# Optimization experiments

Hardware: AMD Instinct MI355X
Metric: run time of the kernel (lower is better)

Reference implementation:

```python
import jax, jax.numpy as jnp
import numpy as np

NUM_SENSORS = 32
STATE_DIM = 2
OBS_DIM = 2 * NUM_SENSORS
T = 4096
LOG2PI = float(np.log(2.0 * np.pi))


def setup_inputs() -> dict:
    key = jax.random.key(0)
    k1, = jax.random.split(key, 1)
    track = jax.random.normal(k1, (T, OBS_DIM), dtype=jnp.float32)
    bias_scales = jnp.ones((2,), dtype=jnp.float32)          # nn.Parameter(torch.ones(2))
    obs_noise = jnp.ones((), dtype=jnp.float32)              # nn.Parameter(torch.tensor(1.0))
    trans_noise = jnp.ones((1,), dtype=jnp.float32)          # nn.Parameter(torch.ones(1))
    transition_param = jnp.ones((2,), dtype=jnp.float32)     # used in forward (diag_embed().flip(0))
    return {
        "track": track,
        "bias_scales": bias_scales,
        "obs_noise": obs_noise,
        "trans_noise": trans_noise,
        "transition_param": transition_param,
    }


def reference(track, bias_scales, obs_noise, trans_noise, transition_param):
    # Gaussian HMM marginal log-likelihood, identical to the funsor sum-product:
    # bias ~ N(0, diag(tile(bias_scales, S)))  (covariance given directly)
    # state_init ~ N(0, I_2)
    # state_t = A^T state_{t-1} + eps,  eps ~ N(0, trans_noise^2 I_2)
    #   with A = diag(transition_param).flip(0), loc = prev @ A = A^T prev
    # obs_t = H^T state_t + bias + nu,  nu ~ N(0, obs_noise^2 I_obs)
    # Bias is folded into an augmented state z = [state, bias] and the whole
    # recursion is a Kalman forward filter (exact marginalization = logaddexp
    # sum-product over Gaussians).
    S = NUM_SENSORS
    sd = STATE_DIM
    od = 2 * S
    d = sd + od

    A = jnp.flip(jnp.diag(transition_param), 0)              # diag_embed().flip(0)
    F_state = A.T                                            # curr_loc = prev @ A
    F = (jnp.zeros((d, d), dtype=track.dtype)
         .at[:sd, :sd].set(F_state)
         .at[sd:, sd:].set(jnp.eye(od, dtype=track.dtype)))  # bias persists
    q = trans_noise[0] ** 2                                  # scale_tril diag -> var
    Q = jnp.zeros((d, d), dtype=track.dtype).at[:sd, :sd].set(q * jnp.eye(sd, dtype=track.dtype))

    # observation_matrix: eye(2).expand(S,2,2).transpose(0,-1).reshape(2, od)
    Ht = jnp.repeat(jnp.eye(sd, dtype=track.dtype), S, axis=0)        # (od, sd)
    C = jnp.concatenate([Ht, jnp.eye(od, dtype=track.dtype)], axis=1)  # (od, d)
    R = (obs_noise ** 2) * jnp.eye(od, dtype=track.dtype)

    bias_var = jnp.tile(bias_scales, S)                      # expand(S,2).reshape(-1)
    P0 = (jnp.zeros((d, d), dtype=track.dtype)
          .at[:sd, :sd].set(jnp.eye(sd, dtype=track.dtype))  # init_dist cov = I_2
          .at[sd:, sd:].set(jnp.diag(bias_var)))
    m0 = jnp.zeros((d,), dtype=track.dtype)

    def step(carry, y):
        m, P, ll = carry
        # predict
        m = F @ m
        P = F @ P @ F.T + Q
        # update
        mu = C @ m
        Smat = C @ P @ C.T + R                               # (od, od)
        L = jnp.linalg.cholesky(Smat)
        r = y - mu
        alpha = jax.scipy.linalg.cho_solve((L, True), r)
        ll = ll + (-0.5 * jnp.dot(r, alpha)
                   - jnp.sum(jnp.log(jnp.diagonal(L)))
                   - 0.5 * od * LOG2PI)
        CP = C @ P                                           # (od, d)
        K = jax.scipy.linalg.cho_solve((L, True), CP).T      # (d, od)
        m = m + K @ r
        P = P - K @ CP
        P = 0.5 * (P + P.T)                                  # keep symmetric
        return (m, P, ll), None

    init = (m0, P0, jnp.zeros((), dtype=track.dtype))
    (_, _, ll), _ = jax.lax.scan(step, init, track)
    return ll
```

## Files before the change

### kernel.cpp

```cpp
#include <hip/hip_runtime.h>

#define TT 4096
#define LOG2PI 1.8378770664093453


struct MRed {
    float a00, a01, a10, a11;
    float b0a, b0b, b1a, b1b;
    float c0, cx, c1;
    float j00, j01, j11;
    float ja, jb, jc, jd;
    float p4d, p4o, p4x, p4e, p4f;
};

struct DRed {
    float g00, g01, g10, g11;
    float ga00, ga01, ga10, ga11;
    float d0a, d0b, d1a, d1b;
    float gc00, gc01, gc10, gc11;
    float clev;
};

struct Elem { float b0, b1, h0, h1, h2, h3, h4, h5, g; };

__device__ __forceinline__ DRed derive(const MRed& M, bool want_clev) {
    DRed D;
    const float cj00 = M.c0 * M.j00 + M.cx * M.j01;
    const float cj01 = M.c0 * M.j01 + M.cx * M.j11;
    const float cj10 = M.cx * M.j00 + M.c1 * M.j01;
    const float cj11 = M.cx * M.j01 + M.c1 * M.j11;
    const float m00 = 1.f + cj00, m01 = cj01, m10 = cj10, m11 = 1.f + cj11;
    const float det = m00 * m11 - m01 * m10;
    const float id = 1.f / det;
    D.g00 = m11 * id; D.g01 = -m01 * id; D.g10 = -m10 * id; D.g11 = m00 * id;
    D.clev = want_clev ? (-0.5f * logf(det)) : 0.f;
    const float CJa0 = M.c0 * M.ja + M.cx * M.jc, CJa1 = M.cx * M.ja + M.c1 * M.jc;
    const float CJb0 = M.c0 * M.jb + M.cx * M.jd, CJb1 = M.cx * M.jb + M.c1 * M.jd;
    const float g0a = -(D.g00 * CJa0 + D.g01 * CJa1);
    const float g1a = -(D.g10 * CJa0 + D.g11 * CJa1);
    const float g0b = -(D.g00 * CJb0 + D.g01 * CJb1);
    const float g1b = -(D.g10 * CJb0 + D.g11 * CJb1);
    D.ga00 = D.g00 * M.a00 + D.g01 * M.a10; D.ga01 = D.g00 * M.a01 + D.g01 * M.a11;
    D.ga10 = D.g10 * M.a00 + D.g11 * M.a10; D.ga11 = D.g10 * M.a01 + D.g11 * M.a11;
    D.d0a = D.g00 * M.b0a + D.g01 * M.b1a + g0a;
    D.d1a = D.g10 * M.b0a + D.g11 * M.b1a + g1a;
    D.d0b = D.g00 * M.b0b + D.g01 * M.b1b + g0b;
    D.d1b = D.g10 * M.b0b + D.g11 * M.b1b + g1b;
    D.gc00 = D.g00 * M.c0 + D.g01 * M.cx; D.gc01 = D.g00 * M.cx + D.g01 * M.c1;
    D.gc10 = D.g10 * M.c0 + D.g11 * M.cx; D.gc11 = D.g10 * M.cx + D.g11 * M.c1;
    return D;
}

__device__ __forceinline__ void mupdate(MRed& M, const DRed& D) {
    const float k00 = M.j00 * D.ga00 + M.j01 * D.ga10, k01 = M.j00 * D.ga01 + M.j01 * D.ga11;
    const float k10 = M.j01 * D.ga00 + M.j11 * D.ga10, k11 = M.j01 * D.ga01 + M.j11 * D.ga11;
    const float V0a = M.j00 * D.d0a + M.j01 * D.d1a + M.ja;
    const float V1a = M.j01 * D.d0a + M.j11 * D.d1a + M.jc;
    const float V0b = M.j00 * D.d0b + M.j01 * D.d1b + M.jb;
    const float V1b = M.j01 * D.d0b + M.j11 * D.d1b + M.jd;
    const float U0a = M.a00 * V0a + M.a10 * V1a, U1a = M.a01 * V0a + M.a11 * V1a;
    const float U0b = M.a00 * V0b + M.a10 * V1b, U1b = M.a01 * V0b + M.a11 * V1b;
    const float Ta0 = M.b0a * k00 + M.b1a * k10 + M.ja * D.ga00 + M.jc * D.ga10;
    const float Ta1 = M.b0a * k01 + M.b1a * k11 + M.ja * D.ga01 + M.jc * D.ga11;
    const float Tb0 = M.b0b * k00 + M.b1b * k10 + M.jb * D.ga00 + M.jd * D.ga10;
    const float Tb1 = M.b0b * k01 + M.b1b * k11 + M.jb * D.ga01 + M.jd * D.ga11;
    const float Eaa = M.b0a * V0a + M.b1a * V1a + M.ja * D.d0a + M.jc * D.d1a;
    const float Eab = M.b0a * V0b + M.b1a * V1b + M.ja * D.d0b + M.jc * D.d1b;
    const float Eba = M.b0b * V0a + M.b1b * V1a + M.jb * D.d0a + M.jd * D.d1a;
    const float Ebb = M.b0b * V0b + M.b1b * V1b + M.jb * D.d0b + M.jd * D.d1b;
    const float nj00 = M.j00 + (M.a00 * k00 + M.a10 * k10);
    const float nj11 = M.j11 + (M.a01 * k01 + M.a11 * k11);
    const float nj01 = M.j01 + 0.5f * ((M.a00 * k01 + M.a10 * k11) + (M.a01 * k00 + M.a11 * k10));
    const float nja = M.ja + 0.5f * (U0a + Ta0);
    const float njc = M.jc + 0.5f * (U1a + Ta1);
    const float njb = M.jb + 0.5f * (U0b + Tb0);
    const float njd = M.jd + 0.5f * (U1b + Tb1);
    const float np4d = M.p4d + Eaa, np4o = M.p4o + Eaa;
    const float np4x = M.p4x + 0.5f * (Eab + Eba);
    const float np4e = M.p4e + Ebb, np4f = M.p4f + Ebb;
    const float ta = M.a00 * D.gc00 + M.a01 * D.gc10, tb = M.a00 * D.gc01 + M.a01 * D.gc11;
    const float tc = M.a10 * D.gc00 + M.a11 * D.gc10, td = M.a10 * D.gc01 + M.a11 * D.gc11;
    const float X00 = ta * M.a00 + tb * M.a01, X01 = ta * M.a10 + tb * M.a11;
    const float X10 = tc * M.a00 + td * M.a01, X11 = tc * M.a10 + td * M.a11;
    const float nc0 = M.c0 + X00, ncx = M.cx + 0.5f * (X01 + X10), nc1 = M.c1 + X11;
    const float na00 = M.a00 * D.ga00 + M.a01 * D.ga10, na01 = M.a00 * D.ga01 + M.a01 * D.ga11;
    const float na10 = M.a10 * D.ga00 + M.a11 * D.ga10, na11 = M.a10 * D.ga01 + M.a11 * D.ga11;
    const float nb0a = M.a00 * D.d0a + M.a01 * D.d1a + M.b0a;
    const float nb1a = M.a10 * D.d0a + M.a11 * D.d1a + M.b1a;
    const float nb0b = M.a00 * D.d0b + M.a01 * D.d1b + M.b0b;
    const float nb1b = M.a10 * D.d0b + M.a11 * D.d1b + M.b1b;
    M.a00 = na00; M.a01 = na01; M.a10 = na10; M.a11 = na11;
    M.b0a = nb0a; M.b0b = nb0b; M.b1a = nb1a; M.b1b = nb1b;
    M.c0 = nc0; M.cx = ncx; M.c1 = nc1;
    M.j00 = nj00; M.j01 = nj01; M.j11 = nj11;
    M.ja = nja; M.jb = njb; M.jc = njc; M.jd = njd;
    M.p4d = np4d; M.p4o = np4o; M.p4x = np4x; M.p4e = np4e; M.p4f = np4f;
}

__device__ __forceinline__ Elem shfl_elem(const Elem& e, int src) {
    Elem r;
    r.b0 = __shfl(e.b0, src, 64); r.b1 = __shfl(e.b1, src, 64);
    r.h0 = __shfl(e.h0, src, 64); r.h1 = __shfl(e.h1, src, 64);
    r.h2 = __shfl(e.h2, src, 64); r.h3 = __shfl(e.h3, src, 64);
    r.h4 = __shfl(e.h4, src, 64); r.h5 = __shfl(e.h5, src, 64);
    r.g  = __shfl(e.g,  src, 64);
    return r;
}

__device__ __forceinline__ Elem compose_red(const MRed& M, const DRed& D,
                                            const Elem& e1, const Elem& e2) {
    const float Jb0 = M.j00 * e1.b0 + M.j01 * e1.b1;
    const float Jb1 = M.j01 * e1.b0 + M.j11 * e1.b1;
    const float Jba = M.ja * e1.b0 + M.jc * e1.b1;
    const float Jbb = M.jb * e1.b0 + M.jd * e1.b1;
    const float Gb0 = D.g00 * e1.b0 + D.g01 * e1.b1;
    const float Gb1 = D.g10 * e1.b0 + D.g11 * e1.b1;
    const float t0 = e1.b0 + M.c0 * e2.h0 + M.cx * e2.h1;
    const float t1 = e1.b1 + M.cx * e2.h0 + M.c1 * e2.h1;
    const float u0 = D.g00 * t0 + D.g01 * t1;
    const float u1 = D.g10 * t0 + D.g11 * t1;
    Elem o;
    o.b0 = M.a00 * u0 + M.a01 * u1 + e2.b0;
    o.b1 = M.a10 * u0 + M.a11 * u1 + e2.b1;
    const float w0 = e2.h0 - Jb0, w1 = e2.h1 - Jb1;
    const float w2 = e2.h2 - Jba, w3 = e2.h3 - Jba;
    const float w4 = e2.h4 - Jbb, w5 = e2.h5 - Jbb;
    o.h0 = e1.h0 + w0 * D.ga00 + w1 * D.ga10;
    o.h1 = e1.h1 + w0 * D.ga01 + w1 * D.ga11;
    o.h2 = e1.h2 + w0 * D.d0a + w1 * D.d1a + w2;
    o.h3 = e1.h3 + w0 * D.d0a + w1 * D.d1a + w3;
    o.h4 = e1.h4 + w0 * D.d0b + w1 * D.d1b + w4;
    o.h5 = e1.h5 + w0 * D.d0b + w1 * D.d1b + w5;
    const float q1 = Jb0 * Gb0 + Jb1 * Gb1;
    const float bil = e2.h0 * Gb0 + e2.h1 * Gb1;
    const float q2 = e2.h0 * (D.gc00 * e2.h0 + D.gc01 * e2.h1)
                   + e2.h1 * (D.gc10 * e2.h0 + D.gc11 * e2.h1);
    o.g = e1.g + e2.g + D.clev - 0.5f * q1 + bil + 0.5f * q2;
    return o;
}

__device__ __forceinline__ MRed m_init(float a0, float a1, float q, float rr,
                                       float& c, float& kpp, float& glc) {
    c = 16.f * q / (rr * (rr + 32.f * q));
    const float s2 = 1.f / rr - 2.f * c;
    kpp = 4.f * q * s2;
    const float om8 = 1.f - 8.f * kpp;
    glc = 2.f * (float)LOG2PI + logf(rr) + logf(rr + 32.f * q);
    MRed M;
    M.a00 = 0.f; M.a01 = om8 * a0; M.a10 = om8 * a1; M.a11 = 0.f;
    M.b0a = -kpp; M.b0b = 0.f; M.b1a = 0.f; M.b1b = -kpp;
    M.c0 = om8 * q; M.cx = 0.f; M.c1 = om8 * q;
    M.j00 = 32.f * a1 * a1 * s2; M.j01 = 0.f; M.j11 = 32.f * a0 * a0 * s2;
    M.ja = 0.f; M.jb = 4.f * a1 * s2; M.jc = 4.f * a0 * s2; M.jd = 0.f;
    const float Sd = 1.f / rr - c, So = -c;
    M.p4d = Sd; M.p4o = So; M.p4x = 0.f; M.p4e = Sd; M.p4f = So;
    return M;
}

__global__ __launch_bounds__(256) void leaf_kernel(const float* __restrict__ track,
                                                   float* __restrict__ ws,
                                                   const float* __restrict__ obs_noise,
                                                   const float* __restrict__ trans_noise,
                                                   const float* __restrict__ tp) {
    __shared__ float zp[256];
    __shared__ float sqp[16], syp[16];
    __shared__ float4 ybar_s[64];
    const int tid = threadIdx.x, w = tid >> 6, l = tid & 63, b = blockIdx.x;
    const float a0 = tp[0], a1 = tp[1];
    const float q = trans_noise[0] * trans_noise[0];
    const float rr = obs_noise[0] * obs_noise[0];
    const float* base = track + (size_t)b * 64 * 64;
    const int g = ((l >> 5) << 1) | (l & 1);
    const bool writer = (l == 0) || (l == 1) || (l == 32) || (l == 33);
    float accz = 0.f, accsq = 0.f, accy2 = 0.f;
#pragma unroll
    for (int it = 0; it < 16; ++it) {
        const int tl = it * 4 + w;
        const float v = base[tl * 64 + l];
        accz += v; accsq += v * v;
        float s = v;
        s += __shfl_xor(s, 2, 64); s += __shfl_xor(s, 4, 64);
        s += __shfl_xor(s, 8, 64); s += __shfl_xor(s, 16, 64);
        if (writer) {
            const float yb = 0.25f * s;
            ((float*)&ybar_s[tl])[g] = yb;
            accy2 += yb * yb;
        }
    }
    zp[tid] = accz;
    float s2 = accsq;
    s2 += __shfl_xor(s2, 2, 64); s2 += __shfl_xor(s2, 4, 64);
    s2 += __shfl_xor(s2, 8, 64); s2 += __shfl_xor(s2, 16, 64);
    if (writer) { sqp[w * 4 + g] = s2; syp[w * 4 + g] = accy2; }
    __syncthreads();
    if (w != 0) return;

    float* slot = ws + b * 96;
    slot[l] = zp[l] + zp[64 + l] + zp[128 + l] + zp[192 + l];
    if (l < 4) {
        slot[64 + l] = sqp[l] + sqp[4 + l] + sqp[8 + l] + sqp[12 + l];
    } else if (l < 8) {
        const int gg = l - 4;
        slot[68 + gg] = syp[gg] + syp[4 + gg] + syp[8 + gg] + syp[12 + gg];
    }

    float c, kpp, glc;
    MRed M = m_init(a0, a1, q, rr, c, kpp, glc);
    const float4 y = ybar_s[l];
    const float irr = 1.f / rr;
    const float bs0 = y.x + y.y, bs1 = y.z + y.w;
    const float v0 = y.x * irr - c * bs0, v1 = y.y * irr - c * bs0;
    const float v2 = y.z * irr - c * bs1, v3 = y.w * irr - c * bs1;
    Elem e;
    e.b0 = kpp * bs0; e.b1 = kpp * bs1;
    e.h0 = 4.f * a1 * (v2 + v3); e.h1 = 4.f * a0 * (v0 + v1);
    e.h2 = v0; e.h3 = v1; e.h4 = v2; e.h5 = v3;
    e.g = -0.5f * (y.x * v0 + y.y * v1 + y.z * v2 + y.w * v3) - glc;

#pragma unroll
    for (int k = 0; k < 6; ++k) {
        const DRed D = derive(M, true);
        const int sA = (2 * l) & 63, sB = (2 * l + 1) & 63;
        const Elem e1 = shfl_elem(e, sA);
        const Elem e2 = shfl_elem(e, sB);
        e = compose_red(M, D, e1, e2);
        mupdate(M, D);
    }
    if (l == 0) {
        float4* eo = (float4*)(slot + 72);
        eo[0] = make_float4(e.b0, e.b1, e.h0, e.h1);
        eo[1] = make_float4(e.h2, e.h3, e.h4, e.h5);
        eo[2] = make_float4(e.g, 0.f, 0.f, 0.f);
    }
}

__global__ __launch_bounds__(64) void final_kernel(const float* __restrict__ ws,
                                                   const float* __restrict__ bias_scales,
                                                   const float* __restrict__ obs_noise,
                                                   const float* __restrict__ trans_noise,
                                                   const float* __restrict__ tp,
                                                   float* __restrict__ out) {
    __shared__ float cst[16];
    const int l = threadIdx.x;
    const float a0 = tp[0], a1 = tp[1];
    const float q = trans_noise[0] * trans_noise[0];
    const float rr = obs_noise[0] * obs_noise[0];
    const float bsc0 = bias_scales[0], bsc1 = bias_scales[1];
    float c, kpp, glc;
    MRed M = m_init(a0, a1, q, rr, c, kpp, glc);
#pragma unroll
    for (int k = 0; k < 6; ++k) { const DRed D = derive(M, false); mupdate(M, D); }

    float zacc = 0.f;
#pragma unroll 8
    for (int b = 0; b < 64; ++b) zacc += ws[b * 96 + l];
    float aux = 0.f;
    if (l < 8) {
        const int off = 64 + l;
#pragma unroll 8
        for (int b = 0; b < 64; ++b) aux += ws[b * 96 + off];
    }

    const float4* ep = (const float4*)(ws + l * 96 + 72);
    const float4 p0 = ep[0], p1 = ep[1], p2 = ep[2];
    Elem e;
    e.b0 = p0.x; e.b1 = p0.y;
    e.h0 = p0.z; e.h1 = p0.w; e.h2 = p1.x; e.h3 = p1.y; e.h4 = p1.z; e.h5 = p1.w;
    e.g = p2.x;

#pragma unroll
    for (int k = 0; k < 6; ++k) {
        const DRed D = derive(M, true);
        const int sA = (2 * l) & 63, sB = (2 * l + 1) & 63;
        const Elem e1 = shfl_elem(e, sA);
        const Elem e2 = shfl_elem(e, sB);
        e = compose_red(M, D, e1, e2);
        mupdate(M, D);
    }

    float sz = zacc, sz2 = zacc * zacc;
    sz += __shfl_xor(sz, 2, 64);  sz2 += __shfl_xor(sz2, 2, 64);
    sz += __shfl_xor(sz, 4, 64);  sz2 += __shfl_xor(sz2, 4, 64);
    sz += __shfl_xor(sz, 8, 64);  sz2 += __shfl_xor(sz2, 8, 64);
    sz += __shfl_xor(sz, 16, 64); sz2 += __shfl_xor(sz2, 16, 64);
    const int g = ((l >> 5) << 1) | (l & 1);
    if (l == 0 || l == 1 || l == 32 || l == 33) { cst[g] = sz; cst[4 + g] = sz2; }
    if (l < 8) cst[8 + l] = aux;
    __syncthreads();

    if (l == 0) {
        float J6[6][6];
        J6[0][0] = M.j00; J6[0][1] = J6[1][0] = M.j01; J6[1][1] = M.j11;
        J6[0][2] = J6[0][3] = J6[2][0] = J6[3][0] = M.ja;
        J6[0][4] = J6[0][5] = J6[4][0] = J6[5][0] = M.jb;
        J6[1][2] = J6[1][3] = J6[2][1] = J6[3][1] = M.jc;
        J6[1][4] = J6[1][5] = J6[4][1] = J6[5][1] = M.jd;
        J6[2][2] = J6[3][3] = M.p4d; J6[2][3] = J6[3][2] = M.p4o;
        J6[2][4] = J6[2][5] = J6[3][4] = J6[3][5] = M.p4x;
        J6[4][2] = J6[5][2] = J6[4][3] = J6[5][3] = M.p4x;
        J6[4][4] = J6[5][5] = M.p4e; J6[4][5] = J6[5][4] = M.p4f;
        const float s[6] = {1.f, 1.f, sqrtf(bsc0), sqrtf(bsc1), sqrtf(bsc0), sqrtf(bsc1)};
        float Mm[6][6];
#pragma unroll
        for (int i = 0; i < 6; ++i)
#pragma unroll
            for (int j = 0; j < 6; ++j)
                Mm[i][j] = ((i == j) ? 1.f : 0.f) + s[i] * s[j] * J6[i][j];
        float Lo[6][6];
#pragma unroll
        for (int i = 0; i < 6; ++i) {
#pragma unroll
            for (int j = 0; j <= i; ++j) {
                float sum = Mm[i][j];
#pragma unroll
                for (int m = 0; m < 6; ++m) if (m < j) sum -= Lo[i][m] * Lo[j][m];
                if (i == j) Lo[i][i] = sqrtf(sum);
                else Lo[i][j] = sum / Lo[j][j];
            }
        }
        float ldet = 0.f;
#pragma unroll
        for (int i = 0; i < 6; ++i) ldet += logf(Lo[i][i]);
        ldet *= 2.f;
        const float hr[6] = {e.h0, e.h1, e.h2, e.h3, e.h4, e.h5};
        float yv[6];
#pragma unroll
        for (int i = 0; i < 6; ++i) {
            float sum = s[i] * hr[i];
#pragma unroll
            for (int m = 0; m < 6; ++m) if (m < i) sum -= Lo[i][m] * yv[m];
            yv[i] = sum / Lo[i][i];
        }
        float qd = 0.f;
#pragma unroll
        for (int i = 0; i < 6; ++i) qd += yv[i] * yv[i];
        double llc = (double)e.g - 0.5 * (double)ldet + 0.5 * (double)qd;

        const float bgv[4] = {bsc0, bsc1, bsc0, bsc1};
        const double r = (double)rr;
        const double T_ = 4096.0;
#pragma unroll
        for (int gg = 0; gg < 4; ++gg) {
            const double b = (double)bgv[gg];
            const double sumz = (double)cst[gg];
            const double sumz2 = (double)cst[4 + gg];
            const double Zp = sumz2 - sumz * sumz / 16.0;
            const double Sqp = (double)cst[8 + gg] - (double)cst[12 + gg];
            llc += -0.5 * Sqp / r
                   + 0.5 * (b / (r * (r + T_ * b))) * Zp
                   - 7.5 * ((T_ - 1.0) * log(r) + log(r + T_ * b))
                   - 7.5 * T_ * LOG2PI;
        }
        out[0] = (float)llc;
    }
}

extern "C" void kernel_launch(void* const* d_in, const int* in_sizes, int n_in,
                              void* d_out, int out_size, void* d_ws, size_t ws_size,
                              hipStream_t stream) {
    const float* track            = (const float*)d_in[0];
    const float* bias_scales      = (const float*)d_in[1];
    const float* obs_noise        = (const float*)d_in[2];
    const float* trans_noise      = (const float*)d_in[3];
    const float* transition_param = (const float*)d_in[4];
    float* ws = (float*)d_ws;
    float* out = (float*)d_out;

    leaf_kernel<<<64, 256, 0, stream>>>(track, ws, obs_noise, trans_noise, transition_param);
    final_kernel<<<1, 64, 0, stream>>>(ws, bias_scales, obs_noise, trans_noise,
                                       transition_param, out);
}
```

Before: 83.90 us.

## Fuse leaf and final kernels using last-block atomic counter

Merges the two launches into one kernel. Each block writes its partial results, then increments a global counter, and the last block to arrive runs the final reduction and scan. The final block now reads the auxiliary sums as float4 loads and reduces them with wave shuffles instead of a serial loop, and the shared-memory staging of the constants becomes register shuffles. A memset of the counter is added on the stream, so the kernel-launch gap is swapped for a memset plus atomic and fence overhead.

Result: no change. 82.97 us (-1.1%).

```diff
diff --git a/kernel.cpp b/kernel.cpp
--- a/kernel.cpp
+++ b/kernel.cpp
@@ -157,14 +157,18 @@
     return M;
 }
 
-__global__ __launch_bounds__(256) void leaf_kernel(const float* __restrict__ track,
-                                                   float* __restrict__ ws,
-                                                   const float* __restrict__ obs_noise,
-                                                   const float* __restrict__ trans_noise,
-                                                   const float* __restrict__ tp) {
+__global__ __launch_bounds__(256) void fused_kernel(const float* __restrict__ track,
+                                                    float* __restrict__ ws,
+                                                    int* __restrict__ counter,
+                                                    const float* __restrict__ bias_scales,
+                                                    const float* __restrict__ obs_noise,
+                                                    const float* __restrict__ trans_noise,
+                                                    const float* __restrict__ tp,
+                                                    float* __restrict__ out) {
     __shared__ float zp[256];
     __shared__ float sqp[16], syp[16];
     __shared__ float4 ybar_s[64];
+    __shared__ int is_last;
     const int tid = threadIdx.x, w = tid >> 6, l = tid & 63, b = blockIdx.x;
     const float a0 = tp[0], a1 = tp[1];
     const float q = trans_noise[0] * trans_noise[0];
@@ -193,102 +197,95 @@
     s2 += __shfl_xor(s2, 8, 64); s2 += __shfl_xor(s2, 16, 64);
     if (writer) { sqp[w * 4 + g] = s2; syp[w * 4 + g] = accy2; }
     __syncthreads();
-    if (w != 0) return;
-
-    float* slot = ws + b * 96;
-    slot[l] = zp[l] + zp[64 + l] + zp[128 + l] + zp[192 + l];
-    if (l < 4) {
-        slot[64 + l] = sqp[l] + sqp[4 + l] + sqp[8 + l] + sqp[12 + l];
-    } else if (l < 8) {
-        const int gg = l - 4;
-        slot[68 + gg] = syp[gg] + syp[4 + gg] + syp[8 + gg] + syp[12 + gg];
-    }
 
     float c, kpp, glc;
     MRed M = m_init(a0, a1, q, rr, c, kpp, glc);
-    const float4 y = ybar_s[l];
-    const float irr = 1.f / rr;
-    const float bs0 = y.x + y.y, bs1 = y.z + y.w;
-    const float v0 = y.x * irr - c * bs0, v1 = y.y * irr - c * bs0;
-    const float v2 = y.z * irr - c * bs1, v3 = y.w * irr - c * bs1;
-    Elem e;
-    e.b0 = kpp * bs0; e.b1 = kpp * bs1;
-    e.h0 = 4.f * a1 * (v2 + v3); e.h1 = 4.f * a0 * (v0 + v1);
-    e.h2 = v0; e.h3 = v1; e.h4 = v2; e.h5 = v3;
-    e.g = -0.5f * (y.x * v0 + y.y * v1 + y.z * v2 + y.w * v3) - glc;
-
-#pragma unroll
-    for (int k = 0; k < 6; ++k) {
-        const DRed D = derive(M, true);
-        const int sA = (2 * l) & 63, sB = (2 * l + 1) & 63;
-        const Elem e1 = shfl_elem(e, sA);
-        const Elem e2 = shfl_elem(e, sB);
-        e = compose_red(M, D, e1, e2);
-        mupdate(M, D);
-    }
-    if (l == 0) {
-        float4* eo = (float4*)(slot + 72);
-        eo[0] = make_float4(e.b0, e.b1, e.h0, e.h1);
-        eo[1] = make_float4(e.h2, e.h3, e.h4, e.h5);
-        eo[2] = make_float4(e.g, 0.f, 0.f, 0.f);
-    }
-}
-
-__global__ __launch_bounds__(64) void final_kernel(const float* __restrict__ ws,
-                                                   const float* __restrict__ bias_scales,
-                                                   const float* __restrict__ obs_noise,
-                                                   const float* __restrict__ trans_noise,
-                                                   const float* __restrict__ tp,
-                                                   float* __restrict__ out) {
-    __shared__ float cst[16];
-    const int l = threadIdx.x;
-    const float a0 = tp[0], a1 = tp[1];
-    const float q = trans_noise[0] * trans_noise[0];
-    const float rr = obs_noise[0] * obs_noise[0];
-    const float bsc0 = bias_scales[0], bsc1 = bias_scales[1];
-    float c, kpp, glc;
-    MRed M = m_init(a0, a1, q, rr, c, kpp, glc);
-#pragma unroll
-    for (int k = 0; k < 6; ++k) { const DRed D = derive(M, false); mupdate(M, D); }
-
-    float zacc = 0.f;
+
+    if (w == 0) {
+        float* slot = ws + b * 96;
+        slot[l] = zp[l] + zp[64 + l] + zp[128 + l] + zp[192 + l];
+        if (l < 4) {
+            slot[64 + l] = sqp[l] + sqp[4 + l] + sqp[8 + l] + sqp[12 + l];
+        } else if (l < 8) {
+            const int gg = l - 4;
+            slot[68 + gg] = syp[gg] + syp[4 + gg] + syp[8 + gg] + syp[12 + gg];
+        }
+        const float4 y = ybar_s[l];
+        const float irr = 1.f / rr;
+        const float bs0 = y.x + y.y, bs1 = y.z + y.w;
+        const float v0 = y.x * irr - c * bs0, v1 = y.y * irr - c * bs0;
+        const float v2 = y.z * irr - c * bs1, v3 = y.w * irr - c * bs1;
+        Elem e;
+        e.b0 = kpp * bs0; e.b1 = kpp * bs1;
+        e.h0 = 4.f * a1 * (v2 + v3); e.h1 = 4.f * a0 * (v0 + v1);
+        e.h2 = v0; e.h3 = v1; e.h4 = v2; e.h5 = v3;
+        e.g = -0.5f * (y.x * v0 + y.y * v1 + y.z * v2 + y.w * v3) - glc;
+#pragma unroll
+        for (int k = 0; k < 6; ++k) {
+            const DRed D = derive(M, true);
+            const Elem e1 = shfl_elem(e, (2 * l) & 63);
+            const Elem e2 = shfl_elem(e, (2 * l + 1) & 63);
+            e = compose_red(M, D, e1, e2);
+            mupdate(M, D);
+        }
+        if (l == 0) {
+            float4* eo = (float4*)(slot + 72);
+            eo[0] = make_float4(e.b0, e.b1, e.h0, e.h1);
+            eo[1] = make_float4(e.h2, e.h3, e.h4, e.h5);
+            eo[2] = make_float4(e.g, 0.f, 0.f, 0.f);
+        }
+    }
+
+    __threadfence();
+    if (tid == 0) is_last = (atomicAdd(counter, 1) == 63);
+    __syncthreads();
+    if (!is_last) return;
+    if (w != 0) return;
+    __threadfence();
+
+    float zl = 0.f;
 #pragma unroll 8
-    for (int b = 0; b < 64; ++b) zacc += ws[b * 96 + l];
-    float aux = 0.f;
-    if (l < 8) {
-        const int off = 64 + l;
-#pragma unroll 8
-        for (int b = 0; b < 64; ++b) aux += ws[b * 96 + off];
-    }
-
-    const float4* ep = (const float4*)(ws + l * 96 + 72);
-    const float4 p0 = ep[0], p1 = ep[1], p2 = ep[2];
+    for (int bb = 0; bb < 64; ++bb) zl += ws[bb * 96 + l];
+
+    const float4* sp = (const float4*)(ws + l * 96 + 64);
+    const float4 q0 = sp[0], q1 = sp[1];
+    const float4 p0 = sp[2], p1 = sp[3], p2 = sp[4];
     Elem e;
     e.b0 = p0.x; e.b1 = p0.y;
     e.h0 = p0.z; e.h1 = p0.w; e.h2 = p1.x; e.h3 = p1.y; e.h4 = p1.z; e.h5 = p1.w;
     e.g = p2.x;
 
+    float axv[8] = {q0.x, q0.y, q0.z, q0.w, q1.x, q1.y, q1.z, q1.w};
+#pragma unroll
+    for (int i = 0; i < 8; ++i) {
+        float t = axv[i];
+        t += __shfl_xor(t, 1, 64); t += __shfl_xor(t, 2, 64); t += __shfl_xor(t, 4, 64);
+        t += __shfl_xor(t, 8, 64); t += __shfl_xor(t, 16, 64); t += __shfl_xor(t, 32, 64);
+        axv[i] = t;
+    }
+
 #pragma unroll
     for (int k = 0; k < 6; ++k) {
         const DRed D = derive(M, true);
-        const int sA = (2 * l) & 63, sB = (2 * l + 1) & 63;
-        const Elem e1 = shfl_elem(e, sA);
-        const Elem e2 = shfl_elem(e, sB);
+        const Elem e1 = shfl_elem(e, (2 * l) & 63);
+        const Elem e2 = shfl_elem(e, (2 * l + 1) & 63);
         e = compose_red(M, D, e1, e2);
         mupdate(M, D);
     }
 
-    float sz = zacc, sz2 = zacc * zacc;
+    float sz = zl, sz2 = zl * zl;
     sz += __shfl_xor(sz, 2, 64);  sz2 += __shfl_xor(sz2, 2, 64);
     sz += __shfl_xor(sz, 4, 64);  sz2 += __shfl_xor(sz2, 4, 64);
     sz += __shfl_xor(sz, 8, 64);  sz2 += __shfl_xor(sz2, 8, 64);
     sz += __shfl_xor(sz, 16, 64); sz2 += __shfl_xor(sz2, 16, 64);
-    const int g = ((l >> 5) << 1) | (l & 1);
-    if (l == 0 || l == 1 || l == 32 || l == 33) { cst[g] = sz; cst[4 + g] = sz2; }
-    if (l < 8) cst[8 + l] = aux;
-    __syncthreads();
+    float csz[4], csz2[4];
+    csz[0] = __shfl(sz, 0, 64);  csz[1] = __shfl(sz, 1, 64);
+    csz[2] = __shfl(sz, 32, 64); csz[3] = __shfl(sz, 33, 64);
+    csz2[0] = __shfl(sz2, 0, 64);  csz2[1] = __shfl(sz2, 1, 64);
+    csz2[2] = __shfl(sz2, 32, 64); csz2[3] = __shfl(sz2, 33, 64);
 
     if (l == 0) {
+        const float bsc0 = bias_scales[0], bsc1 = bias_scales[1];
         float J6[6][6];
         J6[0][0] = M.j00; J6[0][1] = J6[1][0] = M.j01; J6[1][1] = M.j11;
         J6[0][2] = J6[0][3] = J6[2][0] = J6[3][0] = M.ja;
@@ -341,14 +338,14 @@
         const double T_ = 4096.0;
 #pragma unroll
         for (int gg = 0; gg < 4; ++gg) {
-            const double b = (double)bgv[gg];
-            const double sumz = (double)cst[gg];
-            const double sumz2 = (double)cst[4 + gg];
+            const double bb = (double)bgv[gg];
+            const double sumz = (double)csz[gg];
+            const double sumz2 = (double)csz2[gg];
             const double Zp = sumz2 - sumz * sumz / 16.0;
-            const double Sqp = (double)cst[8 + gg] - (double)cst[12 + gg];
+            const double Sqp = (double)axv[gg] - (double)axv[4 + gg];
             llc += -0.5 * Sqp / r
-                   + 0.5 * (b / (r * (r + T_ * b))) * Zp
-                   - 7.5 * ((T_ - 1.0) * log(r) + log(r + T_ * b))
+                   + 0.5 * (bb / (r * (r + T_ * bb))) * Zp
+                   - 7.5 * ((T_ - 1.0) * log(r) + log(r + T_ * bb))
                    - 7.5 * T_ * LOG2PI;
         }
         out[0] = (float)llc;
@@ -364,9 +361,10 @@
     const float* trans_noise      = (const float*)d_in[3];
     const float* transition_param = (const float*)d_in[4];
     float* ws = (float*)d_ws;
+    int* counter = (int*)((char*)d_ws + 24576);
     float* out = (float*)d_out;
 
-    leaf_kernel<<<64, 256, 0, stream>>>(track, ws, obs_noise, trans_noise, transition_param);
-    final_kernel<<<1, 64, 0, stream>>>(ws, bias_scales, obs_noise, trans_noise,
-                                       transition_param, out);
-}
+    hipMemsetAsync(counter, 0, 4, stream);
+    fused_kernel<<<64, 256, 0, stream>>>(track, ws, counter, bias_scales,
+                                         obs_noise, trans_noise, transition_param, out);
+}
```
